# Optimization experiments

Measured on AMD Instinct MI355X. Metric: run time of the kernel, lower is better.

Reference implementation:

```python
import jax, jax.numpy as jnp
import numpy as np

B, N, M = 8, 131072, 64
M_VALID = 48  # trailing padding, matches remove_pad semantics
POSITIVE_IOU = 0.5
NEGATIVE_IOU = 0.3
CLASS_NUM = 1  # hardcoded in RpnTarget.__init__


def _make_boxes(key, shape_prefix, max_wh=64.0, span=1024.0):
    k1, k2, k3, k4 = jax.random.split(key, 4)
    x1 = jax.random.uniform(k1, shape_prefix, minval=0.0, maxval=span)
    y1 = jax.random.uniform(k2, shape_prefix, minval=0.0, maxval=span)
    w = jax.random.uniform(k3, shape_prefix, minval=4.0, maxval=max_wh)
    h = jax.random.uniform(k4, shape_prefix, minval=4.0, maxval=max_wh)
    return jnp.stack([x1, y1, x1 + w, y1 + h], axis=-1)


def setup_inputs() -> dict:
    key = jax.random.key(0)
    ka, kb = jax.random.split(key, 2)
    prior_anchors = _make_boxes(ka, (B, N))                       # [B,N,4]
    boxes = _make_boxes(kb, (B, M), max_wh=128.0)                 # [B,M,4]
    status = jnp.concatenate(
        [jnp.ones((B, M_VALID, 1)), jnp.zeros((B, M - M_VALID, 1))], axis=1
    )
    gt_bboxes = jnp.concatenate([boxes, status], axis=-1)          # [B,M,5]
    gt_class_idxes = jnp.zeros((B, M, 2), dtype=jnp.int32)         # zeroed in call()
    return {
        "prior_anchors": prior_anchors,
        "gt_bboxes": gt_bboxes,
        "gt_class_idxes": gt_class_idxes,
    }


def _bbox_transform(anchors, bboxes):
    # anchors, bboxes: [..., 4] in [x1,y1,x2,y2]
    ax = (anchors[..., 0] + anchors[..., 2]) * 0.5
    ay = (anchors[..., 1] + anchors[..., 3]) * 0.5
    aw = anchors[..., 2] - anchors[..., 0]
    ah = anchors[..., 3] - anchors[..., 1]
    bx = (bboxes[..., 0] + bboxes[..., 2]) * 0.5
    by = (bboxes[..., 1] + bboxes[..., 3]) * 0.5
    bw = bboxes[..., 2] - bboxes[..., 0]
    bh = bboxes[..., 3] - bboxes[..., 1]
    tx = (bx - ax) / aw
    ty = (by - ay) / ah
    tw = jnp.log(bw / aw)
    th = jnp.log(bh / ah)
    return jnp.stack([tx, ty, tw, th], axis=-1)


def _rpn_targets(prior_anchors, gt_bboxes, gt_class_idxes):
    boxes = gt_bboxes[..., :4]                 # [B,M,4]
    valid = gt_bboxes[..., 4] > 0              # [B,M] padding status

    a = prior_anchors[:, :, None, :]           # [B,N,1,4]
    b = boxes[:, None, :, :]                   # [B,1,M,4]
    inter_w = jnp.maximum(jnp.minimum(a[..., 2], b[..., 2]) - jnp.maximum(a[..., 0], b[..., 0]), 0.0)
    inter_h = jnp.maximum(jnp.minimum(a[..., 3], b[..., 3]) - jnp.maximum(a[..., 1], b[..., 1]), 0.0)
    inter = inter_w * inter_h                  # [B,N,M]
    area_a = jnp.maximum(a[..., 2] - a[..., 0], 0.0) * jnp.maximum(a[..., 3] - a[..., 1], 0.0)
    area_b = jnp.maximum(b[..., 2] - b[..., 0], 0.0) * jnp.maximum(b[..., 3] - b[..., 1], 0.0)
    iou = inter / (area_a + area_b - inter)    # [B,N,M]
    # mask out padded gt boxes (equivalent to remove_pad + trailing padding)
    iou = jnp.where(valid[:, None, :], iou, -1.0)

    max_iou = jnp.max(iou, axis=-1)            # [B,N]
    match_idx = jnp.argmax(iou, axis=-1)       # [B,N]
    positive = max_iou >= POSITIVE_IOU
    ignore = (max_iou >= NEGATIVE_IOU) & ~positive

    matched_boxes = jnp.take_along_axis(boxes, match_idx[..., None], axis=1)  # [B,N,4]
    reg = _bbox_transform(prior_anchors, matched_boxes)                        # [B,N,4]

    status = jnp.where(positive, 1.0, jnp.where(ignore, -1.0, 0.0))[..., None]  # [B,N,1]

    # call() zeros gt_class_idxes, so matched class idx is always 0; one_hot depth 1 -> ones
    cls_idx = jnp.take_along_axis(
        jnp.zeros_like(gt_class_idxes)[..., 0], match_idx, axis=1
    )                                                                           # [B,N] int32 zeros
    cls = jax.nn.one_hot(cls_idx, CLASS_NUM, dtype=reg.dtype)                   # [B,N,1]

    regression_targets = jnp.concatenate([reg, status], axis=-1)                # [B,N,5]
    classification_targets = jnp.concatenate([cls, status], axis=-1)            # [B,N,2]
    return regression_targets, classification_targets


def reference(prior_anchors, gt_bboxes, gt_class_idxes):
    return _rpn_targets(prior_anchors, gt_bboxes, gt_class_idxes)
```

## Files before the change

### kernel.cpp

```cpp
#include <hip/hip_runtime.h>


#define BB    8
#define NN    131072
#define MM    64
#define BLK   256
#define NBLK  (NN / BLK)
#define GC    16
#define CELLS (GC * GC)
#define CAP   32

#define WS_BOXES 0
#define WS_AREA  8192
#define WS_CNT   10240
#define WS_LIST  10272
#define WS_LEN   75808

__global__ __launch_bounds__(256) void rpn_build_lists(
    const float* __restrict__ gt, char* __restrict__ ws)
{
    __shared__ float4 sbox[MM];
    __shared__ int    scnt;

    const int b = blockIdx.x;
    const int t = threadIdx.x;

    float4* wboxes = (float4*)(ws + WS_BOXES);
    float*  warea  = (float*)(ws + WS_AREA);
    int*    wcnt   = (int*)(ws + WS_CNT);
    unsigned char* wlist = (unsigned char*)(ws + WS_LIST);
    unsigned char* wlen  = (unsigned char*)(ws + WS_LEN);

    if (t < MM) {
        const float* g = gt + ((size_t)b * MM + t) * 5;
        float x1 = g[0], y1 = g[1], x2 = g[2], y2 = g[3], st = g[4];
        bool valid = (st > 0.0f);
        unsigned long long mask = __ballot(valid);
        int slot = __popcll(mask & ((1ull << t) - 1ull));
        int cntL = __popcll(mask);
        if (t == 0) { scnt = cntL; wcnt[b] = cntL; }
        if (valid) {
            float4 bx = make_float4(x1, y1, x2, y2);
            sbox[slot] = bx;
            wboxes[b * MM + slot] = bx;
            warea[b * MM + slot]  = fmaxf(x2 - x1, 0.0f) * fmaxf(y2 - y1, 0.0f);
        }
        if (t >= cntL) {
            wboxes[b * MM + t] = make_float4(0.f, 0.f, 0.f, 0.f);
            warea[b * MM + t]  = 0.f;
        }
    }
    __syncthreads();

    const int cnt = scnt;
    const int cx = t & (GC - 1), cy = t >> 4;
    const float wx1 = cx * 64.0f, wx2 = wx1 + 128.0f;
    const float wy1 = cy * 64.0f, wy2 = wy1 + 128.0f;

    unsigned long long* lq =
        (unsigned long long*)(wlist + ((size_t)b * CELLS + t) * CAP);
    lq[0] = ~0ull; lq[1] = ~0ull; lq[2] = ~0ull; lq[3] = ~0ull;
    unsigned char* lst = (unsigned char*)lq;

    int len = 0;
    for (int s = 0; s < cnt; ++s) {
        float4 bx = sbox[s];
        if (bx.x <= wx2 && bx.z >= wx1 && bx.y <= wy2 && bx.w >= wy1) {
            if (len < CAP) lst[len] = (unsigned char)s;
            ++len;
        }
    }
    wlen[(size_t)b * CELLS + t] = (unsigned char)len;
}

__global__ __launch_bounds__(BLK) void rpn_target_kernel(
    const float* __restrict__ anchors,
    const float* __restrict__ gt,
    const char* __restrict__ ws,
    float* __restrict__ out)
{
    constexpr float INV = GC / 1024.0f;

    const int t = threadIdx.x;
    const int b = blockIdx.x / NBLK;
    const int n = (blockIdx.x % NBLK) * BLK + t;

    const float4* wboxes = (const float4*)(ws + WS_BOXES) + (size_t)b * MM;
    const float*  warea  = (const float*)(ws + WS_AREA) + (size_t)b * MM;

    const float4 a = ((const float4*)anchors)[(size_t)b * NN + n];

    int cx = (int)(a.x * INV); cx = cx < 0 ? 0 : (cx > GC - 1 ? GC - 1 : cx);
    int cy = (int)(a.y * INV); cy = cy < 0 ? 0 : (cy > GC - 1 ? GC - 1 : cy);
    const int cid = cy * GC + cx;

    const unsigned long long lst8 = *(const unsigned long long*)
        (ws + WS_LIST + ((size_t)b * CELLS + cid) * CAP);
    const int len = ((const unsigned char*)(ws + WS_LEN))[(size_t)b * CELLS + cid];
    const int cnt = ((const int*)(ws + WS_CNT))[b];

    const float area_a = fmaxf(a.z - a.x, 0.0f) * fmaxf(a.w - a.y, 0.0f);

    float best  = 0.0f;
    int   bslot = 0;

    float iou[8]; int id[8];
    #pragma unroll
    for (int j = 0; j < 8; ++j) {
        const int raw = (int)((lst8 >> (8 * j)) & 0xFFull);
        const int idx = raw & 63;
        id[j] = idx;
        const float4 bb = wboxes[idx];
        const float  ab = warea[idx];
        float iw = fmaxf(fminf(a.z, bb.z) - fmaxf(a.x, bb.x), 0.0f);
        float ih = fmaxf(fminf(a.w, bb.w) - fmaxf(a.y, bb.y), 0.0f);
        float inter = iw * ih;
        inter = (raw != 255) ? inter : 0.0f;
        float denom = (area_a + ab) - inter;
        iou[j] = inter / denom;
    }
    #pragma unroll
    for (int j = 0; j < 8; ++j)
        if (iou[j] > best) { best = iou[j]; bslot = id[j]; }

    if (__any(len > 8)) {
        const unsigned char* gl = (const unsigned char*)
            (ws + WS_LIST + ((size_t)b * CELLS + cid) * CAP);
        const int L = (len <= CAP) ? len : 0;
        for (int j = 8; j < L; ++j) {
            const int idx = gl[j];
            const float4 bb = wboxes[idx];
            float iw = fmaxf(fminf(a.z, bb.z) - fmaxf(a.x, bb.x), 0.0f);
            float ih = fmaxf(fminf(a.w, bb.w) - fmaxf(a.y, bb.y), 0.0f);
            float inter = iw * ih;
            if (inter > 0.0f) {
                float denom = (area_a + warea[idx]) - inter;
                float iou = inter / denom;
                if (iou > best) { best = iou; bslot = idx; }
            }
        }
    }
    if (__any(len > CAP)) {
        if (len > CAP) {
            best = 0.0f; bslot = 0;
            for (int j = 0; j < cnt; ++j) {
                const float4 bb = wboxes[j];
                float iw = fmaxf(fminf(a.z, bb.z) - fmaxf(a.x, bb.x), 0.0f);
                float ih = fmaxf(fminf(a.w, bb.w) - fmaxf(a.y, bb.y), 0.0f);
                float inter = iw * ih;
                if (inter > 0.0f) {
                    float denom = (area_a + warea[j]) - inter;
                    float iou = inter / denom;
                    if (iou > best) { best = iou; bslot = j; }
                }
            }
        }
    }

    const float status = (best >= 0.5f) ? 1.0f : ((best >= 0.3f) ? -1.0f : 0.0f);

    float4 mb;
    if (cnt > 0) {
        mb = wboxes[bslot];
    } else {
        const float* g0 = gt + (size_t)b * MM * 5;
        mb = make_float4(g0[0], g0[1], g0[2], g0[3]);
    }

    const float aw  = a.z - a.x;
    const float ah  = a.w - a.y;
    const float rw  = __builtin_amdgcn_rcpf(aw);
    const float rh  = __builtin_amdgcn_rcpf(ah);
    const float tx  = ((mb.x + mb.z) * 0.5f - (a.x + a.z) * 0.5f) * rw;
    const float ty  = ((mb.y + mb.w) * 0.5f - (a.y + a.w) * 0.5f) * rh;
    const float LN2 = 0.69314718055994531f;
    const float tw  = __builtin_amdgcn_logf((mb.z - mb.x) * rw) * LN2;
    const float th  = __builtin_amdgcn_logf((mb.w - mb.y) * rh) * LN2;

    const size_t gid = (size_t)b * NN + n;

    float* r = out + gid * 5;
    r[0] = tx; r[1] = ty; r[2] = tw; r[3] = th; r[4] = status;

    float2* c = (float2*)(out + (size_t)BB * NN * 5) + gid;
    *c = make_float2(1.0f, status);
}

extern "C" void kernel_launch(void* const* d_in, const int* in_sizes, int n_in,
                              void* d_out, int out_size, void* d_ws, size_t ws_size,
                              hipStream_t stream) {
    const float* anchors = (const float*)d_in[0];
    const float* gt      = (const float*)d_in[1];

    float* out = (float*)d_out;
    char*  ws  = (char*)d_ws;

    hipLaunchKernelGGL(rpn_build_lists, dim3(BB), dim3(256), 0, stream, gt, ws);
    hipLaunchKernelGGL(rpn_target_kernel, dim3(BB * NBLK), dim3(BLK), 0, stream,
                       anchors, gt, ws, out);
}
```

Baseline: 28.70 us.

## Shrink cell lists to 8 entries, compute areas inline, coalesce regression stores via LDS

The per-cell candidate list now holds only 8 packed indices in a single u64, and any cell with more than 8 candidates falls back to a full scan over all boxes instead of walking a 32-entry list. The separate area array is removed; box areas are computed inline, and the matched box is carried in registers instead of being re-read by index. Regression outputs are staged in shared memory and written as coalesced rows instead of strided 5-float stores per thread. The workspace shrinks and the list-building kernel does less work, but overflowing cells now pay for a full scan, and the staging adds a barrier.

```diff
diff --git a/kernel.cpp b/kernel.cpp
--- a/kernel.cpp
+++ b/kernel.cpp
@@ -8,13 +8,14 @@
 #define NBLK  (NN / BLK)
 #define GC    16
 #define CELLS (GC * GC)
-#define CAP   32
 
 #define WS_BOXES 0
-#define WS_AREA  8192
-#define WS_CNT   10240
-#define WS_LIST  10272
-#define WS_LEN   75808
+#define WS_CNT   8192
+#define WS_L8    8224
+#define WS_LEN   24608
+
+typedef unsigned long long u64;
+typedef unsigned char u8;
 
 __global__ __launch_bounds__(256) void rpn_build_lists(
     const float* __restrict__ gt, char* __restrict__ ws)
@@ -26,16 +27,15 @@
     const int t = threadIdx.x;
 
     float4* wboxes = (float4*)(ws + WS_BOXES);
-    float*  warea  = (float*)(ws + WS_AREA);
     int*    wcnt   = (int*)(ws + WS_CNT);
-    unsigned char* wlist = (unsigned char*)(ws + WS_LIST);
-    unsigned char* wlen  = (unsigned char*)(ws + WS_LEN);
+    u64*    wl8    = (u64*)(ws + WS_L8);
+    u8*     wlen   = (u8*)(ws + WS_LEN);
 
     if (t < MM) {
         const float* g = gt + ((size_t)b * MM + t) * 5;
         float x1 = g[0], y1 = g[1], x2 = g[2], y2 = g[3], st = g[4];
         bool valid = (st > 0.0f);
-        unsigned long long mask = __ballot(valid);
+        u64 mask = __ballot(valid);
         int slot = __popcll(mask & ((1ull << t) - 1ull));
         int cntL = __popcll(mask);
         if (t == 0) { scnt = cntL; wcnt[b] = cntL; }
@@ -43,12 +43,9 @@
             float4 bx = make_float4(x1, y1, x2, y2);
             sbox[slot] = bx;
             wboxes[b * MM + slot] = bx;
-            warea[b * MM + slot]  = fmaxf(x2 - x1, 0.0f) * fmaxf(y2 - y1, 0.0f);
         }
-        if (t >= cntL) {
+        if (t >= cntL)
             wboxes[b * MM + t] = make_float4(0.f, 0.f, 0.f, 0.f);
-            warea[b * MM + t]  = 0.f;
-        }
     }
     __syncthreads();
 
@@ -57,20 +54,20 @@
     const float wx1 = cx * 64.0f, wx2 = wx1 + 128.0f;
     const float wy1 = cy * 64.0f, wy2 = wy1 + 128.0f;
 
-    unsigned long long* lq =
-        (unsigned long long*)(wlist + ((size_t)b * CELLS + t) * CAP);
-    lq[0] = ~0ull; lq[1] = ~0ull; lq[2] = ~0ull; lq[3] = ~0ull;
-    unsigned char* lst = (unsigned char*)lq;
-
+    u64 l8 = ~0ull;
     int len = 0;
     for (int s = 0; s < cnt; ++s) {
         float4 bx = sbox[s];
         if (bx.x <= wx2 && bx.z >= wx1 && bx.y <= wy2 && bx.w >= wy1) {
-            if (len < CAP) lst[len] = (unsigned char)s;
+            if (len < 8) {
+                const int sh = 8 * len;
+                l8 = (l8 & ~(0xFFull << sh)) | ((u64)s << sh);
+            }
             ++len;
         }
     }
-    wlen[(size_t)b * CELLS + t] = (unsigned char)len;
+    wl8[(size_t)b * CELLS + t]  = l8;
+    wlen[(size_t)b * CELLS + t] = (u8)len;
 }
 
 __global__ __launch_bounds__(BLK) void rpn_target_kernel(
@@ -81,12 +78,13 @@
 {
     constexpr float INV = GC / 1024.0f;
 
+    __shared__ float sreg[BLK * 5];
+
     const int t = threadIdx.x;
     const int b = blockIdx.x / NBLK;
     const int n = (blockIdx.x % NBLK) * BLK + t;
 
     const float4* wboxes = (const float4*)(ws + WS_BOXES) + (size_t)b * MM;
-    const float*  warea  = (const float*)(ws + WS_AREA) + (size_t)b * MM;
 
     const float4 a = ((const float4*)anchors)[(size_t)b * NN + n];
 
@@ -94,75 +92,54 @@
     int cy = (int)(a.y * INV); cy = cy < 0 ? 0 : (cy > GC - 1 ? GC - 1 : cy);
     const int cid = cy * GC + cx;
 
-    const unsigned long long lst8 = *(const unsigned long long*)
-        (ws + WS_LIST + ((size_t)b * CELLS + cid) * CAP);
-    const int len = ((const unsigned char*)(ws + WS_LEN))[(size_t)b * CELLS + cid];
-    const int cnt = ((const int*)(ws + WS_CNT))[b];
+    const u64 lst8 = ((const u64*)(ws + WS_L8))[(size_t)b * CELLS + cid];
+    const int cnt  = ((const int*)(ws + WS_CNT))[b];
 
     const float area_a = fmaxf(a.z - a.x, 0.0f) * fmaxf(a.w - a.y, 0.0f);
 
-    float best  = 0.0f;
-    int   bslot = 0;
+    float  best = 0.0f;
+    float4 mb   = wboxes[0];
 
-    float iou[8]; int id[8];
+    float  iou[8];
+    float4 cb[8];
     #pragma unroll
     for (int j = 0; j < 8; ++j) {
         const int raw = (int)((lst8 >> (8 * j)) & 0xFFull);
         const int idx = raw & 63;
-        id[j] = idx;
         const float4 bb = wboxes[idx];
-        const float  ab = warea[idx];
+        cb[j] = bb;
         float iw = fmaxf(fminf(a.z, bb.z) - fmaxf(a.x, bb.x), 0.0f);
         float ih = fmaxf(fminf(a.w, bb.w) - fmaxf(a.y, bb.y), 0.0f);
         float inter = iw * ih;
         inter = (raw != 255) ? inter : 0.0f;
+        float ab = fmaxf(bb.z - bb.x, 0.0f) * fmaxf(bb.w - bb.y, 0.0f);
         float denom = (area_a + ab) - inter;
         iou[j] = inter / denom;
     }
     #pragma unroll
     for (int j = 0; j < 8; ++j)
-        if (iou[j] > best) { best = iou[j]; bslot = id[j]; }
+        if (iou[j] > best) { best = iou[j]; mb = cb[j]; }
 
-    if (__any(len > 8)) {
-        const unsigned char* gl = (const unsigned char*)
-            (ws + WS_LIST + ((size_t)b * CELLS + cid) * CAP);
-        const int L = (len <= CAP) ? len : 0;
-        for (int j = 8; j < L; ++j) {
-            const int idx = gl[j];
-            const float4 bb = wboxes[idx];
-            float iw = fmaxf(fminf(a.z, bb.z) - fmaxf(a.x, bb.x), 0.0f);
-            float ih = fmaxf(fminf(a.w, bb.w) - fmaxf(a.y, bb.y), 0.0f);
-            float inter = iw * ih;
-            if (inter > 0.0f) {
-                float denom = (area_a + warea[idx]) - inter;
-                float iou = inter / denom;
-                if (iou > best) { best = iou; bslot = idx; }
-            }
-        }
-    }
-    if (__any(len > CAP)) {
-        if (len > CAP) {
-            best = 0.0f; bslot = 0;
+    if (__any(((lst8 >> 56) & 0xFFull) != 0xFFull)) {
+        const int len = ((const u8*)(ws + WS_LEN))[(size_t)b * CELLS + cid];
+        if (len > 8) {
+            best = 0.0f; mb = wboxes[0];
             for (int j = 0; j < cnt; ++j) {
                 const float4 bb = wboxes[j];
                 float iw = fmaxf(fminf(a.z, bb.z) - fmaxf(a.x, bb.x), 0.0f);
                 float ih = fmaxf(fminf(a.w, bb.w) - fmaxf(a.y, bb.y), 0.0f);
                 float inter = iw * ih;
-                if (inter > 0.0f) {
-                    float denom = (area_a + warea[j]) - inter;
-                    float iou = inter / denom;
-                    if (iou > best) { best = iou; bslot = j; }
-                }
+                float ab = fmaxf(bb.z - bb.x, 0.0f) * fmaxf(bb.w - bb.y, 0.0f);
+                float denom = (area_a + ab) - inter;
+                float iou = inter / denom;
+                if (iou > best) { best = iou; mb = bb; }
             }
         }
     }
 
     const float status = (best >= 0.5f) ? 1.0f : ((best >= 0.3f) ? -1.0f : 0.0f);
 
-    float4 mb;
-    if (cnt > 0) {
-        mb = wboxes[bslot];
-    } else {
+    if (cnt == 0) {
         const float* g0 = gt + (size_t)b * MM * 5;
         mb = make_float4(g0[0], g0[1], g0[2], g0[3]);
     }
@@ -177,11 +154,19 @@
     const float tw  = __builtin_amdgcn_logf((mb.z - mb.x) * rw) * LN2;
     const float th  = __builtin_amdgcn_logf((mb.w - mb.y) * rh) * LN2;
 
+    sreg[t * 5 + 0] = tx;
+    sreg[t * 5 + 1] = ty;
+    sreg[t * 5 + 2] = tw;
+    sreg[t * 5 + 3] = th;
+    sreg[t * 5 + 4] = status;
+    __syncthreads();
+
+    const size_t regbase = ((size_t)b * NN + (size_t)(blockIdx.x % NBLK) * BLK) * 5;
+    #pragma unroll
+    for (int k = 0; k < 5; ++k)
+        out[regbase + (size_t)k * BLK + t] = sreg[k * BLK + t];
+
     const size_t gid = (size_t)b * NN + n;
-
-    float* r = out + gid * 5;
-    r[0] = tx; r[1] = ty; r[2] = tw; r[3] = th; r[4] = status;
-
     float2* c = (float2*)(out + (size_t)BB * NN * 5) + gid;
     *c = make_float2(1.0f, status);
 }
```

New measurement: 27.34 us. 1.05x faster.
